# Performance work log

Hardware: AMD Instinct MI355X
Metric: run time of the kernel (lower is better)

Reference implementation:

```python
import jax, jax.numpy as jnp
import numpy as np

S, B, D = 2048, 2, 1024
H, KV = 16, 4
HD = D // H          # 64
N_REP = H // KV      # 4
EPS = 1e-5
THETA = 10000.0
SCALE = D ** -0.5    # qk_norm_scale = 0.03125 (use_qk_norm path)


def rms_norm(x, w, eps=EPS):
    return x / jnp.sqrt(jnp.mean(x * x, axis=-1, keepdims=True) + eps) * w


def rotate_half(x):
    x1, x2 = jnp.split(x, 2, axis=-1)
    return jnp.concatenate((-x2, x1), axis=-1)


def rope_tables(seq_len, dim, theta=THETA):
    inv_freq = 1.0 / (theta ** (jnp.arange(0, dim, 2, dtype=jnp.float32) / dim))
    t = jnp.arange(seq_len, dtype=jnp.float32)
    freqs = jnp.outer(t, inv_freq)                 # [S, dim/2]
    emb = jnp.concatenate((freqs, freqs), axis=-1)  # [S, dim]
    return jnp.cos(emb), jnp.sin(emb)


def setup_inputs() -> dict:
    key = jax.random.key(0)
    ks = jax.random.split(key, 16)
    s = lambda fan_in: fan_in ** -0.5
    return {
        "x": jax.random.normal(ks[0], (S, B, D), jnp.float32),
        "norm1_w": jnp.ones((D,), jnp.float32),
        "wq": jax.random.normal(ks[1], (D, H * HD), jnp.float32) * s(D),
        "bq": jnp.zeros((H * HD,), jnp.float32),
        "wk": jax.random.normal(ks[2], (D, KV * HD), jnp.float32) * s(D),
        "bk": jnp.zeros((KV * HD,), jnp.float32),
        "wv": jax.random.normal(ks[3], (D, KV * HD), jnp.float32) * s(D),
        "bv": jnp.zeros((KV * HD,), jnp.float32),
        "qn_w": jnp.ones((HD,), jnp.float32),
        "kn_w": jnp.ones((HD,), jnp.float32),
        "wo": jax.random.normal(ks[4], (D, D), jnp.float32) * s(D),
        "bo": jnp.zeros((D,), jnp.float32),
        "norm2_w": jnp.ones((D,), jnp.float32),
        "w1": jax.random.normal(ks[5], (D, 4 * D), jnp.float32) * s(D),
        "b1": jnp.zeros((4 * D,), jnp.float32),
        "w2": jax.random.normal(ks[6], (4 * D, D), jnp.float32) * s(4 * D),
        "b2": jnp.zeros((D,), jnp.float32),
    }


def reference(x, norm1_w, wq, bq, wk, bk, wv, bv, qn_w, kn_w, wo, bo,
              norm2_w, w1, b1, w2, b2):
    # x: [S, B, D] (seq-first, TE convention)
    residual = x
    h = rms_norm(x, norm1_w)
    q = (h @ wq + bq).reshape(S, B, H, HD).transpose(1, 2, 0, 3)    # [B,H,S,HD]
    k = (h @ wk + bk).reshape(S, B, KV, HD).transpose(1, 2, 0, 3)   # [B,KV,S,HD]
    v = (h @ wv + bv).reshape(S, B, KV, HD).transpose(1, 2, 0, 3)
    # GQA: repeat_interleave over head dim
    k = jnp.repeat(k, N_REP, axis=1)  # [B,H,S,HD]
    v = jnp.repeat(v, N_REP, axis=1)
    # per-head QK RMSNorm
    q = rms_norm(q, qn_w)
    k = rms_norm(k, kn_w)
    # RoPE
    cos, sin = rope_tables(S, HD)          # [S,HD] each
    cos = cos[None, None]                  # [1,1,S,HD]
    sin = sin[None, None]
    q = q * cos + rotate_half(q) * sin
    k = k * cos + rotate_half(k) * sin
    # attention with explicit causal mask
    scores = jnp.einsum('bhsd,bhtd->bhst', q, k) * SCALE
    causal = jnp.triu(jnp.ones((S, S), bool), k=1)
    scores = jnp.where(causal, -jnp.inf, scores)
    attn = jax.nn.softmax(scores, axis=-1)
    out = jnp.einsum('bhst,bhtd->bhsd', attn, v)       # [B,H,S,HD]
    out = out.transpose(0, 2, 1, 3).reshape(B, S, D)   # [B,S,D]
    out = out.transpose(1, 0, 2)                       # [S,B,D]
    out = out @ wo + bo
    x = residual + out
    # MLP block (RMSNorm + GELU MLP)
    residual = x
    h2 = rms_norm(x, norm2_w)
    h2 = jax.nn.gelu(h2 @ w1 + b1, approximate=False) @ w2 + b2
    return residual + h2
```

## Files before the change

### kernel.cpp

```cpp
#include <hip/hip_runtime.h>
#include <hip/hip_bf16.h>
#include <math.h>

#define S_LEN 2048
#define BATCH 2
#define DMODEL 1024
#define NH 16
#define NKV 4
#define HDIM 64
#define EPS 1e-5f
#define MROWS (S_LEN*BATCH)
#define QSCALE (0.03125f * 1.44269504088896f)

#define AS1 __attribute__((address_space(1)))
#define AS3 __attribute__((address_space(3)))

typedef __attribute__((ext_vector_type(8))) short bf8_t;
typedef __attribute__((ext_vector_type(4))) float f4_t;
typedef _Float16 __attribute__((ext_vector_type(8))) h8_t;
typedef _Float16 __attribute__((ext_vector_type(4))) h4_t;

#define MFMA16(a,b,c) __builtin_amdgcn_mfma_f32_16x16x16f16(a,b,c,0,0,0)

__device__ __forceinline__ float exp2_fast(float x){ return __builtin_exp2f(x); }

__device__ __forceinline__ unsigned short f2bf(float f){
  __hip_bfloat16 b = __float2bfloat16(f);
  return __builtin_bit_cast(unsigned short, b);
}
__device__ __forceinline__ float bf2f(unsigned short u){
  return __builtin_bit_cast(float, (unsigned)u << 16);
}
__device__ __forceinline__ float gelu_f(float x){
  return 0.5f * x * (1.0f + erff(x * 0.7071067811865475f));
}

__global__ __launch_bounds__(256) void prep_k(const float* __restrict__ wq, const float* __restrict__ wk,
                                              const float* __restrict__ wv, const float* __restrict__ wo,
                                              const float* __restrict__ w1, const float* __restrict__ w2,
                                              __hip_bfloat16* __restrict__ wqkv_t, __hip_bfloat16* __restrict__ wo_t,
                                              __hip_bfloat16* __restrict__ w1_t,   __hip_bfloat16* __restrict__ w2_t,
                                              const float* __restrict__ x, const float* __restrict__ n1w,
                                              __hip_bfloat16* __restrict__ h){
  if (blockIdx.x < 10752){
    __shared__ float t[32][33];
    int b = blockIdx.x;
    const float* src; __hip_bfloat16* dst; int N, stride, nx;
    if (b < 1024)      { src=wq; dst=wqkv_t;               N=1024; stride=1024; nx=32;  }
    else if (b < 1280) { b-=1024; src=wk; dst=wqkv_t+1024*1024; N=256; stride=1024; nx=8; }
    else if (b < 1536) { b-=1280; src=wv; dst=wqkv_t+1280*1024; N=256; stride=1024; nx=8; }
    else if (b < 2560) { b-=1536; src=wo; dst=wo_t;        N=1024; stride=1024; nx=32;  }
    else if (b < 6656) { b-=2560; src=w1; dst=w1_t;        N=4096; stride=1024; nx=128; }
    else               { b-=6656; src=w2; dst=w2_t;        N=1024; stride=4096; nx=32;  }
    int n0 = (b % nx)*32, k0 = (b / nx)*32;
    int tx = threadIdx.x & 31, ty = threadIdx.x >> 5;
    #pragma unroll
    for (int i = 0; i < 4; ++i)
      t[ty*4+i][tx] = src[(size_t)(k0+ty*4+i)*N + n0 + tx];
    __syncthreads();
    #pragma unroll
    for (int i = 0; i < 4; ++i)
      dst[(size_t)(n0+ty*4+i)*stride + k0 + tx] = __float2bfloat16(t[tx][ty*4+i]);
  } else {
    __shared__ float sm[5];
    size_t row = blockIdx.x - 10752;
    const float4* xr = (const float4*)(x + row * DMODEL);
    float4 v = xr[threadIdx.x];
    float ss = v.x*v.x + v.y*v.y + v.z*v.z + v.w*v.w;
    #pragma unroll
    for (int off = 32; off; off >>= 1) ss += __shfl_down(ss, off);
    if ((threadIdx.x & 63) == 0) sm[threadIdx.x >> 6] = ss;
    __syncthreads();
    if (threadIdx.x == 0) sm[4] = rsqrtf((sm[0]+sm[1]+sm[2]+sm[3]) * (1.0f/DMODEL) + EPS);
    __syncthreads();
    float r = sm[4];
    float4 wv4 = ((const float4*)n1w)[threadIdx.x];
    ushort4 ob;
    ob.x = f2bf(v.x*r*wv4.x); ob.y = f2bf(v.y*r*wv4.y);
    ob.z = f2bf(v.z*r*wv4.z); ob.w = f2bf(v.w*r*wv4.w);
    ((ushort4*)(h + row * DMODEL))[threadIdx.x] = ob;
  }
}

template<int EPI, bool DB>
__global__ __launch_bounds__(256) void mgemm_k(const __hip_bfloat16* __restrict__ A,
                                               const __hip_bfloat16* __restrict__ Wt,
                                               const float* __restrict__ bias,
                                               __hip_bfloat16* __restrict__ Cb,
                                               int N, int Kstride, int kLen){
  __shared__ __align__(16) __hip_bfloat16 As[DB?2:1][8192];
  __shared__ __align__(16) __hip_bfloat16 Bs[DB?2:1][8192];
  const int tid = threadIdx.x;
  const int w = tid >> 6, l = tid & 63;
  const int lr = l & 15, lc = l >> 4;

  const unsigned gx = gridDim.x, gy = gridDim.y;
  unsigned hb  = (blockIdx.z * gy + blockIdx.y) * gx + blockIdx.x;
  unsigned cpx = (gx * gy * gridDim.z) >> 3;
  unsigned role = (hb & 7u) * cpx + (hb >> 3);
  unsigned bxi = role % gx; unsigned t2 = role / gx;
  unsigned byi = t2 % gy;   unsigned bzi = t2 / gy;

  const int bm = byi * 128, bn = bxi * 128;
  const int wm = (w >> 1) * 64, wn = (w & 1) * 64;
  const int kOff = bzi * kLen;

  const __hip_bfloat16* Ag = A  + (size_t)(bm + 2*w*16 + lr)*Kstride + kOff + lc*8;
  const __hip_bfloat16* Bg = Wt + (size_t)(bn + 2*w*16 + lr)*Kstride + kOff + lc*8;

  f4_t acc[4][4] = {};

  auto stage = [&](int buf, int k0){
    #pragma unroll
    for (int rg = 0; rg < 2; ++rg)
      #pragma unroll
      for (int j = 0; j < 2; ++j){
        __builtin_amdgcn_global_load_lds((const AS1 void*)(Ag + rg*16*(size_t)Kstride + k0 + j*32),
                                         (AS3 void*)(&As[buf][(2*w+rg)*1024 + j*512 + l*8]), 16, 0, 0);
        __builtin_amdgcn_global_load_lds((const AS1 void*)(Bg + rg*16*(size_t)Kstride + k0 + j*32),
                                         (AS3 void*)(&Bs[buf][(2*w+rg)*1024 + j*512 + l*8]), 16, 0, 0);
      }
  };

  auto compute = [&](int buf){
    #pragma unroll
    for (int s = 0; s < 2; ++s){
      bf8_t af[4], bfr[4];
      #pragma unroll
      for (int mi = 0; mi < 4; ++mi)
        af[mi] = *(const bf8_t*)(&As[buf][((wm>>4)+mi)*1024 + s*512 + l*8]);
      #pragma unroll
      for (int ni = 0; ni < 4; ++ni)
        bfr[ni] = *(const bf8_t*)(&Bs[buf][((wn>>4)+ni)*1024 + s*512 + l*8]);
      #pragma unroll
      for (int mi = 0; mi < 4; ++mi)
        #pragma unroll
        for (int ni = 0; ni < 4; ++ni)
          acc[mi][ni] = __builtin_amdgcn_mfma_f32_16x16x32_bf16(af[mi], bfr[ni], acc[mi][ni], 0, 0, 0);
    }
  };

  if constexpr (DB){
    const int nt = kLen >> 6;
    stage(0, 0);
    asm volatile("s_waitcnt vmcnt(0)" ::: "memory");
    __builtin_amdgcn_s_barrier();
    int cur = 0;
    for (int t = 0; t < nt; ++t){
      if (t + 1 < nt) stage(cur ^ 1, (t + 1) << 6);
      compute(cur);
      asm volatile("s_waitcnt vmcnt(0)" ::: "memory");
      __builtin_amdgcn_s_barrier();
      cur ^= 1;
    }
  } else {
    for (int k0 = 0; k0 < kLen; k0 += 64){
      __syncthreads();
      stage(0, k0);
      __syncthreads();
      compute(0);
    }
  }

  __hip_bfloat16* Cp = (EPI == 3) ? (Cb + (size_t)bzi * ((size_t)MROWS * N)) : Cb;

  #pragma unroll
  for (int ni = 0; ni < 4; ++ni){
    int col = bn + wn + ni*16 + lr;
    float bb = (EPI == 3) ? 0.0f : bias[col];
    #pragma unroll
    for (int mi = 0; mi < 4; ++mi){
      #pragma unroll
      for (int r = 0; r < 4; ++r){
        int row = bm + wm + mi*16 + lc*4 + r;
        size_t off = (size_t)row * N + col;
        float v = acc[mi][ni][r] + bb;
        if (EPI == 1) Cp[off] = __float2bfloat16(gelu_f(v));
        else          Cp[off] = __float2bfloat16(v);
      }
    }
  }
}

template<int NS>
__global__ __launch_bounds__(256) void reduce_k(const unsigned short* __restrict__ P,
                                                const float* __restrict__ bias,
                                                const float* __restrict__ res,
                                                float* __restrict__ out, int N){
  size_t i = ((size_t)blockIdx.x*256 + threadIdx.x) * 4;
  int col = (int)(i % (size_t)N);
  size_t stride = (size_t)MROWS * N;
  float a0=0,a1=0,a2=0,a3=0;
  #pragma unroll
  for (int p = 0; p < NS; ++p){
    ushort4 u = *(const ushort4*)(P + p*stride + i);
    a0 += bf2f(u.x); a1 += bf2f(u.y); a2 += bf2f(u.z); a3 += bf2f(u.w);
  }
  float4 bb = *(const float4*)(bias + col);
  float4 r4 = *(const float4*)(res + i);
  float4 o = make_float4(a0+bb.x+r4.x, a1+bb.y+r4.y, a2+bb.z+r4.z, a3+bb.w+r4.w);
  *(float4*)(out + i) = o;
}

template<int NS>
__global__ __launch_bounds__(256) void redn_k(const unsigned short* __restrict__ P,
                                              const float* __restrict__ bias,
                                              const float* __restrict__ res,
                                              const float* __restrict__ nw,
                                              float* __restrict__ x1,
                                              __hip_bfloat16* __restrict__ h){
  __shared__ float sm[5];
  size_t row = blockIdx.x;
  size_t i = row * DMODEL + threadIdx.x*4;
  size_t stride = (size_t)MROWS * DMODEL;
  float4 bb = *(const float4*)(bias + threadIdx.x*4);
  float4 r4 = *(const float4*)(res + i);
  float4 v = make_float4(bb.x+r4.x, bb.y+r4.y, bb.z+r4.z, bb.w+r4.w);
  #pragma unroll
  for (int p = 0; p < NS; ++p){
    ushort4 u = *(const ushort4*)(P + p*stride + i);
    v.x += bf2f(u.x); v.y += bf2f(u.y); v.z += bf2f(u.z); v.w += bf2f(u.w);
  }
  *(float4*)(x1 + i) = v;
  float ss = v.x*v.x + v.y*v.y + v.z*v.z + v.w*v.w;
  #pragma unroll
  for (int off = 32; off; off >>= 1) ss += __shfl_down(ss, off);
  if ((threadIdx.x & 63) == 0) sm[threadIdx.x >> 6] = ss;
  __syncthreads();
  if (threadIdx.x == 0) sm[4] = rsqrtf((sm[0]+sm[1]+sm[2]+sm[3]) * (1.0f/DMODEL) + EPS);
  __syncthreads();
  float r = sm[4];
  float4 wv = ((const float4*)nw)[threadIdx.x];
  ushort4 ob;
  ob.x = f2bf(v.x*r*wv.x); ob.y = f2bf(v.y*r*wv.y);
  ob.z = f2bf(v.z*r*wv.z); ob.w = f2bf(v.w*r*wv.w);
  ((ushort4*)(h + row * DMODEL))[threadIdx.x] = ob;
}

__global__ __launch_bounds__(64) void rope2_k(const unsigned short* __restrict__ P,
                                              const float* __restrict__ bq, const float* __restrict__ bk,
                                              const float* __restrict__ qw, const float* __restrict__ kw,
                                              _Float16* __restrict__ qo, _Float16* __restrict__ ko){
  const int s = blockIdx.x;
  const int y = blockIdx.y;
  const int b = y / 20, r0 = y % 20;
  const bool isQ = (r0 < 16);
  const int hh = isQ ? r0 : (r0 - 16);
  const int col0 = isQ ? hh*64 : 1024 + hh*64;
  const int lane = threadIdx.x;
  const size_t pstride = (size_t)MROWS * 1536;
  size_t off = ((size_t)s * BATCH + b) * 1536 + col0 + lane;
  float v = bf2f(P[off]) + bf2f(P[off + pstride])
          + (isQ ? bq[hh*64 + lane] : bk[hh*64 + lane]);
  float ss = v * v;
  #pragma unroll
  for (int m = 32; m; m >>= 1) ss += __shfl_xor(ss, m);
  float rr = rsqrtf(ss * (1.0f/64.0f) + EPS);
  v = v * rr * (isQ ? qw[lane] : kw[lane]);
  int i = lane & 31;
  float invf = powf(10000.0f, -((float)(2*i)) * (1.0f/64.0f));
  float ang = (float)s * invf;
  float c, sn;
  sincosf(ang, &sn, &c);
  float partner = __shfl_xor(v, 32);
  float rh = (lane < 32) ? -partner : partner;
  float o = (v * c + rh * sn) * (isQ ? QSCALE : 1.0f);
  _Float16* outp = isQ ? (qo + (((size_t)b * NH  + hh) * S_LEN + s) * 64 + lane)
                       : (ko + (((size_t)b * NKV + hh) * S_LEN + s) * 64 + lane);
  *outp = (_Float16)o;
}

__global__ __launch_bounds__(256) void vcast_k(const unsigned short* __restrict__ P,
                                               const float* __restrict__ bv,
                                               _Float16* __restrict__ Vt){
  __shared__ float t[64][65];
  const int s0 = blockIdx.x * 64;
  const int bkv = blockIdx.y;
  const int b = bkv >> 2, kv = bkv & 3;
  const int tid = threadIdx.x;
  const size_t pstride = (size_t)MROWS * 1536;
  #pragma unroll
  for (int i = 0; i < 16; ++i){
    int idx = tid + 256*i;
    int sl = idx >> 6, d = idx & 63;
    size_t off = ((size_t)(s0+sl)*BATCH + b)*1536 + 1280 + kv*64 + d;
    t[d][sl] = bf2f(P[off]) + bf2f(P[off + pstride]) + bv[kv*64 + d];
  }
  __syncthreads();
  #pragma unroll
  for (int i = 0; i < 16; ++i){
    int idx = tid + 256*i;
    int d = idx >> 6, sl = idx & 63;
    Vt[((size_t)bkv*64 + d)*S_LEN + s0 + sl] = (_Float16)t[d][sl];
  }
}

__global__ __launch_bounds__(256) void attn2_k(const _Float16* __restrict__ Q,
                                               const _Float16* __restrict__ K,
                                               const _Float16* __restrict__ Vt,
                                               __hip_bfloat16* __restrict__ AO){
  __shared__ __align__(16) _Float16 Ks[8*512];
  __shared__ __align__(16) _Float16 Vs[8*512];
  const int bh = blockIdx.x;
  const int qb = (gridDim.y - 1) - blockIdx.y;
  const int b = bh >> 4, h = bh & 15;
  const int kvh = h >> 2;
  const int tid = threadIdx.x;
  const int w = tid >> 6, l = tid & 63;
  const int lr = l & 15, quad = l >> 4;

  const _Float16* qp = Q + ((size_t)bh * S_LEN + qb*64 + w*16 + lr) * 64;
  h8_t qf0 = *(const h8_t*)(qp + quad*8);
  h8_t qf1 = *(const h8_t*)(qp + 32 + quad*8);

  const _Float16* kbase = K  + (size_t)(b*NKV + kvh) * S_LEN * 64;
  const _Float16* vbase = Vt + (size_t)(b*NKV + kvh) * 64 * S_LEN;

  f4_t Od[4] = {};
  float m_i = -3.0e38f, l_i = 0.0f;

  for (int kt = 0; kt <= qb; ++kt){
    __syncthreads();
    #pragma unroll
    for (int ii = 0; ii < 4; ++ii){
      int i = w*4 + ii;
      if (i < 8){
        int cc = i >> 1, dh = i & 1;
        const _Float16* src = kbase + (size_t)(kt*64 + cc*16 + lr)*64 + dh*32 + quad*8;
        __builtin_amdgcn_global_load_lds((const AS1 void*)src, (AS3 void*)(Ks + i*512), 16, 0, 0);
      } else {
        int j = i - 8;
        int dd = j >> 1, cc32 = j & 1;
        const _Float16* src = vbase + (size_t)(dd*16 + lr)*S_LEN + kt*64 + cc32*32 + quad*8;
        __builtin_amdgcn_global_load_lds((const AS1 void*)src, (AS3 void*)(Vs + j*512), 16, 0, 0);
      }
    }
    __syncthreads();

    const bool diag = (kt == qb);
    f4_t sc[4];
    #pragma unroll
    for (int nc2 = 0; nc2 < 4; ++nc2){
      if (diag && nc2 > w){
        sc[nc2][0] = -1.0e30f; sc[nc2][1] = -1.0e30f;
        sc[nc2][2] = -1.0e30f; sc[nc2][3] = -1.0e30f;
        continue;
      }
      f4_t a = {};
      h8_t k0 = *(const h8_t*)(Ks + (nc2*2+0)*512 + l*8);
      h8_t k1 = *(const h8_t*)(Ks + (nc2*2+1)*512 + l*8);
      a = __builtin_amdgcn_mfma_f32_16x16x32_f16(k0, qf0, a, 0, 0, 0);
      a = __builtin_amdgcn_mfma_f32_16x16x32_f16(k1, qf1, a, 0, 0, 0);
      if (diag && nc2 == w){
        #pragma unroll
        for (int r = 0; r < 4; ++r)
          if (quad*4 + r > lr) a[r] = -1.0e30f;
      }
      sc[nc2] = a;
    }

    float mx = sc[0][0];
    #pragma unroll
    for (int nc2 = 0; nc2 < 4; ++nc2)
      #pragma unroll
      for (int r = 0; r < 4; ++r) mx = fmaxf(mx, sc[nc2][r]);
    mx = fmaxf(mx, __shfl_xor(mx, 16));
    mx = fmaxf(mx, __shfl_xor(mx, 32));
    float nm = fmaxf(mx, m_i);
    float alpha = exp2_fast(m_i - nm);
    m_i = nm;
    float rs = 0.0f;
    h4_t pf[4];
    #pragma unroll
    for (int nc2 = 0; nc2 < 4; ++nc2)
      #pragma unroll
      for (int r = 0; r < 4; ++r){
        float e = exp2_fast(sc[nc2][r] - nm);
        rs += e;
        pf[nc2][r] = (_Float16)e;
      }
    rs += __shfl_xor(rs, 16);
    rs += __shfl_xor(rs, 32);
    l_i = l_i * alpha + rs;
    #pragma unroll
    for (int dd = 0; dd < 4; ++dd)
      #pragma unroll
      for (int r = 0; r < 4; ++r) Od[dd][r] *= alpha;

    #pragma unroll
    for (int dd = 0; dd < 4; ++dd)
      #pragma unroll
      for (int nc2 = 0; nc2 < 4; ++nc2){
        if (diag && nc2 > w) continue;
        h4_t vf = *(const h4_t*)(Vs + (dd*2 + (nc2>>1))*512
                                 + (((nc2&1)*2 + (quad>>1))*16 + lr)*8 + (quad&1)*4);
        Od[dd] = MFMA16(vf, pf[nc2], Od[dd]);
      }
  }

  float inv = 1.0f / l_i;
  #pragma unroll
  for (int dd = 0; dd < 4; ++dd){
    ushort4 w4;
    w4.x = f2bf(Od[dd][0]*inv); w4.y = f2bf(Od[dd][1]*inv);
    w4.z = f2bf(Od[dd][2]*inv); w4.w = f2bf(Od[dd][3]*inv);
    size_t sg = (size_t)qb*64 + w*16 + lr;
    *(ushort4*)(AO + (sg*BATCH + b)*DMODEL + h*64 + dd*16 + quad*4) = w4;
  }
}

extern "C" void kernel_launch(void* const* d_in, const int* in_sizes, int n_in,
                              void* d_out, int out_size, void* d_ws, size_t ws_size,
                              hipStream_t stream){
  const float* x   = (const float*)d_in[0];
  const float* n1w = (const float*)d_in[1];
  const float* wq  = (const float*)d_in[2];
  const float* bq  = (const float*)d_in[3];
  const float* wk  = (const float*)d_in[4];
  const float* bk  = (const float*)d_in[5];
  const float* wv  = (const float*)d_in[6];
  const float* bv  = (const float*)d_in[7];
  const float* qnw = (const float*)d_in[8];
  const float* knw = (const float*)d_in[9];
  const float* wo  = (const float*)d_in[10];
  const float* bo  = (const float*)d_in[11];
  const float* n2w = (const float*)d_in[12];
  const float* w1  = (const float*)d_in[13];
  const float* b1  = (const float*)d_in[14];
  const float* w2  = (const float*)d_in[15];
  const float* b2  = (const float*)d_in[16];
  float* out = (float*)d_out;

  char* p = (char*)d_ws;
  auto carve = [&](size_t bytes)->char*{ char* r = p; p += (bytes + 255) & ~(size_t)255; return r; };
  __hip_bfloat16* h_bf   = (__hip_bfloat16*)carve((size_t)MROWS*DMODEL*2);
  __hip_bfloat16* ao_bf  = (__hip_bfloat16*)carve((size_t)MROWS*DMODEL*2);
  __hip_bfloat16* mid_bf = (__hip_bfloat16*)carve((size_t)MROWS*4096*2);
  __hip_bfloat16* wqkv_t = (__hip_bfloat16*)carve((size_t)1536*1024*2);
  __hip_bfloat16* wo_t   = (__hip_bfloat16*)carve((size_t)1024*1024*2);
  __hip_bfloat16* w1_t   = (__hip_bfloat16*)carve((size_t)4096*1024*2);
  __hip_bfloat16* w2_t   = (__hip_bfloat16*)carve((size_t)1024*4096*2);
  char* scratch = carve((size_t)2*MROWS*1536*2);
  __hip_bfloat16* qkv_p = (__hip_bfloat16*)scratch;
  __hip_bfloat16* ps    = (__hip_bfloat16*)scratch;
  _Float16* q_f  = (_Float16*)carve((size_t)BATCH*NH *S_LEN*64*2);
  _Float16* k_f  = (_Float16*)carve((size_t)BATCH*NKV*S_LEN*64*2);
  _Float16* vt_f = (_Float16*)carve((size_t)BATCH*NKV*64*S_LEN*2);
  float* x1   = (float*)carve((size_t)MROWS*DMODEL*4);

  prep_k<<<10752 + MROWS, 256, 0, stream>>>(wq, wk, wv, wo, w1, w2,
                                            wqkv_t, wo_t, w1_t, w2_t, x, n1w, h_bf);

  mgemm_k<3,true><<<dim3(12, 32, 2), 256, 0, stream>>>(h_bf, wqkv_t, nullptr, qkv_p, 1536, 1024, 512);

  rope2_k<<<dim3(S_LEN, BATCH*20), 64, 0, stream>>>((const unsigned short*)qkv_p, bq, bk, qnw, knw, q_f, k_f);
  vcast_k<<<dim3(S_LEN/64, BATCH*NKV), 256, 0, stream>>>((const unsigned short*)qkv_p, bv, vt_f);
  attn2_k<<<dim3(BATCH*NH, S_LEN/64), 256, 0, stream>>>(q_f, k_f, vt_f, ao_bf);

  mgemm_k<3,true><<<dim3(8, 32, 2), 256, 0, stream>>>(ao_bf, wo_t, nullptr, ps, 1024, 1024, 512);
  redn_k<2><<<MROWS, 256, 0, stream>>>((const unsigned short*)ps, bo, x, n2w, x1, h_bf);

  mgemm_k<1,true><<<dim3(32, 32, 1), 256, 0, stream>>>(h_bf, w1_t, b1, mid_bf, 4096, 1024, 1024);

  mgemm_k<3,false><<<dim3(8, 32, 2), 256, 0, stream>>>(mid_bf, w2_t, nullptr, ps, 1024, 4096, 2048);
  reduce_k<2><<<4096, 256, 0, stream>>>((const unsigned short*)ps, b2, x1, out, 1024);
}
```

Baseline: 425.1 us.

## Use 256x256-tile 512-thread GEMM for MLP layers with 4-way split-K down-projection

Adds a 256x256 output-tile GEMM kernel with 8 waves and double-buffered LDS (64KB per buffer pair), used for the MLP up-projection and the down-projection. The down-projection now splits K four ways (kLen 1024) instead of two, and the reduce kernel sums four bf16 partials; scratch is enlarged to hold them. The w2 GEMM also moves from the single-buffered path to double buffering. Larger tiles raise arithmetic intensity and cut global traffic per FLOP, but they reduce occupancy, launch fewer blocks (256 for each MLP GEMM), and add extra partial-sum traffic in the reduce.

New measurement: 427.6 us. No clear change (+0.6%).

```diff
diff --git a/kernel.cpp b/kernel.cpp
--- a/kernel.cpp
+++ b/kernel.cpp
@@ -82,14 +82,14 @@
   }
 }
 
-template<int EPI, bool DB>
+template<int EPI>
 __global__ __launch_bounds__(256) void mgemm_k(const __hip_bfloat16* __restrict__ A,
                                                const __hip_bfloat16* __restrict__ Wt,
                                                const float* __restrict__ bias,
                                                __hip_bfloat16* __restrict__ Cb,
                                                int N, int Kstride, int kLen){
-  __shared__ __align__(16) __hip_bfloat16 As[DB?2:1][8192];
-  __shared__ __align__(16) __hip_bfloat16 Bs[DB?2:1][8192];
+  __shared__ __align__(16) __hip_bfloat16 As[2][8192];
+  __shared__ __align__(16) __hip_bfloat16 Bs[2][8192];
   const int tid = threadIdx.x;
   const int w = tid >> 6, l = tid & 63;
   const int lr = l & 15, lc = l >> 4;
@@ -140,26 +140,17 @@
     }
   };
 
-  if constexpr (DB){
-    const int nt = kLen >> 6;
-    stage(0, 0);
+  const int nt = kLen >> 6;
+  stage(0, 0);
+  asm volatile("s_waitcnt vmcnt(0)" ::: "memory");
+  __builtin_amdgcn_s_barrier();
+  int cur = 0;
+  for (int t = 0; t < nt; ++t){
+    if (t + 1 < nt) stage(cur ^ 1, (t + 1) << 6);
+    compute(cur);
     asm volatile("s_waitcnt vmcnt(0)" ::: "memory");
     __builtin_amdgcn_s_barrier();
-    int cur = 0;
-    for (int t = 0; t < nt; ++t){
-      if (t + 1 < nt) stage(cur ^ 1, (t + 1) << 6);
-      compute(cur);
-      asm volatile("s_waitcnt vmcnt(0)" ::: "memory");
-      __builtin_amdgcn_s_barrier();
-      cur ^= 1;
-    }
-  } else {
-    for (int k0 = 0; k0 < kLen; k0 += 64){
-      __syncthreads();
-      stage(0, k0);
-      __syncthreads();
-      compute(0);
-    }
+    cur ^= 1;
   }
 
   __hip_bfloat16* Cp = (EPI == 3) ? (Cb + (size_t)bzi * ((size_t)MROWS * N)) : Cb;
@@ -170,6 +161,96 @@
     float bb = (EPI == 3) ? 0.0f : bias[col];
     #pragma unroll
     for (int mi = 0; mi < 4; ++mi){
+      #pragma unroll
+      for (int r = 0; r < 4; ++r){
+        int row = bm + wm + mi*16 + lc*4 + r;
+        size_t off = (size_t)row * N + col;
+        float v = acc[mi][ni][r] + bb;
+        if (EPI == 1) Cp[off] = __float2bfloat16(gelu_f(v));
+        else          Cp[off] = __float2bfloat16(v);
+      }
+    }
+  }
+}
+
+template<int EPI>
+__global__ __launch_bounds__(512) void mgemm256_k(const __hip_bfloat16* __restrict__ A,
+                                                  const __hip_bfloat16* __restrict__ Wt,
+                                                  const float* __restrict__ bias,
+                                                  __hip_bfloat16* __restrict__ Cb,
+                                                  int N, int Kstride, int kLen){
+  __shared__ __align__(16) __hip_bfloat16 As[2][16384];
+  __shared__ __align__(16) __hip_bfloat16 Bs[2][16384];
+  const int tid = threadIdx.x;
+  const int w = tid >> 6, l = tid & 63;
+  const int lr = l & 15, lc = l >> 4;
+
+  const unsigned gx = gridDim.x, gy = gridDim.y;
+  unsigned hb  = (blockIdx.z * gy + blockIdx.y) * gx + blockIdx.x;
+  unsigned cpx = (gx * gy * gridDim.z) >> 3;
+  unsigned role = (hb & 7u) * cpx + (hb >> 3);
+  unsigned bxi = role % gx; unsigned t2 = role / gx;
+  unsigned byi = t2 % gy;   unsigned bzi = t2 / gy;
+
+  const int bm = byi * 256, bn = bxi * 256;
+  const int wm = (w >> 2) * 128, wn = (w & 3) * 64;
+  const int kOff = bzi * kLen;
+
+  const __hip_bfloat16* Ag = A  + (size_t)(bm + 2*w*16 + lr)*Kstride + kOff + lc*8;
+  const __hip_bfloat16* Bg = Wt + (size_t)(bn + 2*w*16 + lr)*Kstride + kOff + lc*8;
+
+  f4_t acc[8][4] = {};
+
+  auto stage = [&](int buf, int k0){
+    #pragma unroll
+    for (int rg = 0; rg < 2; ++rg)
+      #pragma unroll
+      for (int j = 0; j < 2; ++j){
+        __builtin_amdgcn_global_load_lds((const AS1 void*)(Ag + rg*16*(size_t)Kstride + k0 + j*32),
+                                         (AS3 void*)(&As[buf][(2*w+rg)*1024 + j*512 + l*8]), 16, 0, 0);
+        __builtin_amdgcn_global_load_lds((const AS1 void*)(Bg + rg*16*(size_t)Kstride + k0 + j*32),
+                                         (AS3 void*)(&Bs[buf][(2*w+rg)*1024 + j*512 + l*8]), 16, 0, 0);
+      }
+  };
+
+  auto compute = [&](int buf){
+    #pragma unroll
+    for (int s = 0; s < 2; ++s){
+      bf8_t bfr[4];
+      #pragma unroll
+      for (int ni = 0; ni < 4; ++ni)
+        bfr[ni] = *(const bf8_t*)(&Bs[buf][((wn>>4)+ni)*1024 + s*512 + l*8]);
+      #pragma unroll
+      for (int mi = 0; mi < 8; ++mi){
+        bf8_t af = *(const bf8_t*)(&As[buf][((wm>>4)+mi)*1024 + s*512 + l*8]);
+        #pragma unroll
+        for (int ni = 0; ni < 4; ++ni)
+          acc[mi][ni] = __builtin_amdgcn_mfma_f32_16x16x32_bf16(af, bfr[ni], acc[mi][ni], 0, 0, 0);
+      }
+    }
+  };
+
+  const int nt = kLen >> 6;
+  stage(0, 0);
+  asm volatile("s_waitcnt vmcnt(0)" ::: "memory");
+  __builtin_amdgcn_s_barrier();
+  int cur = 0;
+  for (int t = 0; t < nt; ++t){
+    if (t + 1 < nt) stage(cur ^ 1, (t + 1) << 6);
+    compute(cur);
+    asm volatile("s_waitcnt vmcnt(0)" ::: "memory");
+    __builtin_amdgcn_s_barrier();
+    cur ^= 1;
+  }
+
+  __hip_bfloat16* Cp = (EPI == 3) ? (Cb + (size_t)bzi * ((size_t)MROWS * N)) : Cb;
+
+  #pragma unroll
+  for (int ni = 0; ni < 4; ++ni){
+    int col = bn + wn + ni*16 + lr;
+    float bb = (EPI == 3) ? 0.0f : bias[col];
+    #pragma unroll
+    for (int mi = 0; mi < 8; ++mi){
       #pragma unroll
       for (int r = 0; r < 4; ++r){
         int row = bm + wm + mi*16 + lc*4 + r;
@@ -440,7 +521,7 @@
   __hip_bfloat16* wo_t   = (__hip_bfloat16*)carve((size_t)1024*1024*2);
   __hip_bfloat16* w1_t   = (__hip_bfloat16*)carve((size_t)4096*1024*2);
   __hip_bfloat16* w2_t   = (__hip_bfloat16*)carve((size_t)1024*4096*2);
-  char* scratch = carve((size_t)2*MROWS*1536*2);
+  char* scratch = carve((size_t)4*MROWS*DMODEL*2);
   __hip_bfloat16* qkv_p = (__hip_bfloat16*)scratch;
   __hip_bfloat16* ps    = (__hip_bfloat16*)scratch;
   _Float16* q_f  = (_Float16*)carve((size_t)BATCH*NH *S_LEN*64*2);
@@ -451,17 +532,17 @@
   prep_k<<<10752 + MROWS, 256, 0, stream>>>(wq, wk, wv, wo, w1, w2,
                                             wqkv_t, wo_t, w1_t, w2_t, x, n1w, h_bf);
 
-  mgemm_k<3,true><<<dim3(12, 32, 2), 256, 0, stream>>>(h_bf, wqkv_t, nullptr, qkv_p, 1536, 1024, 512);
+  mgemm_k<3><<<dim3(12, 32, 2), 256, 0, stream>>>(h_bf, wqkv_t, nullptr, qkv_p, 1536, 1024, 512);
 
   rope2_k<<<dim3(S_LEN, BATCH*20), 64, 0, stream>>>((const unsigned short*)qkv_p, bq, bk, qnw, knw, q_f, k_f);
   vcast_k<<<dim3(S_LEN/64, BATCH*NKV), 256, 0, stream>>>((const unsigned short*)qkv_p, bv, vt_f);
   attn2_k<<<dim3(BATCH*NH, S_LEN/64), 256, 0, stream>>>(q_f, k_f, vt_f, ao_bf);
 
-  mgemm_k<3,true><<<dim3(8, 32, 2), 256, 0, stream>>>(ao_bf, wo_t, nullptr, ps, 1024, 1024, 512);
+  mgemm_k<3><<<dim3(8, 32, 2), 256, 0, stream>>>(ao_bf, wo_t, nullptr, ps, 1024, 1024, 512);
   redn_k<2><<<MROWS, 256, 0, stream>>>((const unsigned short*)ps, bo, x, n2w, x1, h_bf);
 
-  mgemm_k<1,true><<<dim3(32, 32, 1), 256, 0, stream>>>(h_bf, w1_t, b1, mid_bf, 4096, 1024, 1024);
-
-  mgemm_k<3,false><<<dim3(8, 32, 2), 256, 0, stream>>>(mid_bf, w2_t, nullptr, ps, 1024, 4096, 2048);
-  reduce_k<2><<<4096, 256, 0, stream>>>((const unsigned short*)ps, b2, x1, out, 1024);
-}
+  mgemm256_k<1><<<dim3(16, 16, 1), 512, 0, stream>>>(h_bf, w1_t, b1, mid_bf, 4096, 1024, 1024);
+
+  mgemm256_k<3><<<dim3(4, 16, 4), 512, 0, stream>>>(mid_bf, w2_t, nullptr, ps, 1024, 4096, 1024);
+  reduce_k<4><<<4096, 256, 0, stream>>>((const unsigned short*)ps, b2, x1, out, 1024);
+}
```
